# Kernel tuning notes

Measured on AMD Instinct MI355X. Metric: run time of the kernel, lower is better.

## Reference

```python
import jax, jax.numpy as jnp
import numpy as np

B, T, D = 16, 2048, 256
WINDOW = 128


def setup_inputs() -> dict:
    key = jax.random.key(0)
    ks = jax.random.split(key, 6)
    scale = 1.0 / np.sqrt(D)
    return {
        "x": jax.random.normal(ks[0], (B, T, D), dtype=jnp.float32),
        "Wq": jax.random.normal(ks[1], (D, D), dtype=jnp.float32) * scale,
        "Wk": jax.random.normal(ks[2], (D, D), dtype=jnp.float32) * scale,
        "Wv": jax.random.normal(ks[3], (D, D), dtype=jnp.float32) * scale,
        "Wo": jax.random.normal(ks[4], (D, D), dtype=jnp.float32) * scale,
        "w_bias": jax.random.normal(ks[5], (T, T), dtype=jnp.float32) * 0.1,
        "window": WINDOW,
    }


def reference(x, Wq, Wk, Wv, Wo, w_bias, window):
    # x: [B,T,D]; w_bias: [T,T] learned pairwise position bias.
    T_ = x.shape[1]
    q = jnp.einsum("btd,de->bte", x, Wq)
    k = jnp.einsum("btd,de->bte", x, Wk)
    v = jnp.einsum("btd,de->bte", x, Wv)

    # AFT-Local: bias is zeroed outside the local band |t - t'| < window,
    # but ALL positions still contribute (with bias 0) to the weighted sum.
    idx = jnp.arange(T_)
    band = jnp.abs(idx[:, None] - idx[None, :]) < window  # [T,T] bool
    w_local = jnp.where(band, w_bias, 0.0)

    # Stable exponentials: the num/den ratio is invariant to per-row shifts
    # of w and per-(b,d) shifts of k.
    w_stable = w_local - jnp.max(w_local, axis=1, keepdims=True)
    k_stable = k - jnp.max(k, axis=1, keepdims=True)
    expw = jnp.exp(w_stable)  # [T,T]
    expk = jnp.exp(k_stable)  # [B,T,D]

    num = jnp.einsum("ts,bsd->btd", expw, expk * v)
    den = jnp.einsum("ts,bsd->btd", expw, expk)
    y = jax.nn.sigmoid(q) * (num / den)
    return jnp.einsum("btd,de->bte", y, Wo)
```

## Files before the change

kernel.cpp:

```cpp
#include <hip/hip_runtime.h>
#include <math.h>

#define B_ 16
#define T_ 2048
#define D_ 256
#define W_ 128
#define M_ (B_*T_)

typedef __attribute__((ext_vector_type(8))) short bf16x8;
typedef __attribute__((ext_vector_type(4))) float f32x4;
typedef unsigned short u16;

static __device__ __forceinline__ u16 f32_bf16_rne(float f) {
    unsigned int u = __float_as_uint(f);
    u += 0x7FFF + ((u >> 16) & 1);
    return (u16)(u >> 16);
}
static __device__ __forceinline__ float bf16_f32(u16 h) {
    return __uint_as_float(((unsigned int)h) << 16);
}
static __device__ __forceinline__ void gload_lds16(const u16* g, u16* l) {
    __builtin_amdgcn_global_load_lds(
        (const __attribute__((address_space(1))) void*)g,
        (__attribute__((address_space(3))) void*)l, 16, 0, 0);
}

__global__ __launch_bounds__(256) void aft_split_wT(
    const float* __restrict__ Wq, const float* __restrict__ Wk,
    const float* __restrict__ Wv, const float* __restrict__ Wo,
    u16* __restrict__ Wth, u16* __restrict__ Wkl)
{
    __shared__ alignas(16) u16 Th[64][72];
    __shared__ alignas(16) u16 Tl[64][72];
    const float* Ws[4] = {Wq, Wk, Wv, Wo};
    const int mat = blockIdx.x;
    const float* W = Ws[mat];
    const int k0 = (blockIdx.y & 3) * 64;
    const int n0 = (blockIdx.y >> 2) * 64;
    const int tid = threadIdx.x;

    #pragma unroll
    for (int p = 0; p < 4; ++p) {
        const int k = p * 16 + (tid >> 4);
        const int n = (tid & 15) * 4;
        float4 v = *(const float4*)&W[(size_t)(k0 + k) * 256 + n0 + n];
        float vv[4] = {v.x, v.y, v.z, v.w};
        #pragma unroll
        for (int e = 0; e < 4; ++e) {
            u16 h = f32_bf16_rne(vv[e]);
            Th[n + e][k] = h;
            Tl[n + e][k] = f32_bf16_rne(vv[e] - bf16_f32(h));
        }
    }
    __syncthreads();

    const int n  = tid >> 2;
    const int kc = (tid & 3) * 16;
    size_t ob = ((size_t)mat * 256 + n0 + n) * 256 + k0 + kc;
    *(uint4*)&Wth[ob]     = *(const uint4*)&Th[n][kc];
    *(uint4*)&Wth[ob + 8] = *(const uint4*)&Th[n][kc + 8];
    if (mat == 1) {
        size_t ol = ((size_t)(n0 + n)) * 256 + k0 + kc;
        *(uint4*)&Wkl[ol]     = *(const uint4*)&Tl[n][kc];
        *(uint4*)&Wkl[ol + 8] = *(const uint4*)&Tl[n][kc + 8];
    }
}

__global__ void aft_ewb(const float* __restrict__ wb, u16* __restrict__ EWb)
{
    const int t = blockIdx.x;
    const int j = threadIdx.x;
    const int s = (t & ~63) - 128 + j;
    const int dlt = s - t;
    float v = 0.f;
    if (s >= 0 && s < T_ && dlt > -W_ && dlt < W_)
        v = expf(wb[(size_t)t * T_ + s]) - 1.0f;
    EWb[(size_t)t * 320 + j] = f32_bf16_rne(v);
}

__global__ __launch_bounds__(256, 3) void aft_qkv_mfma(
    const float* __restrict__ x,
    const u16* __restrict__ Wth, const u16* __restrict__ Wkl,
    u16* __restrict__ ekT, u16* __restrict__ sigqT)
{
    __shared__ alignas(16) u16 sm[12288];
    u16* Ah = sm;
    u16* Al = sm + 2048;
    u16* Bs = sm + 4096;
    u16* Tr = sm;

    const int tid  = threadIdx.x;
    const int row0 = blockIdx.x * 64;
    const int col0 = blockIdx.y * 64;
    const int b    = row0 >> 11;
    const int t0g  = row0 & (T_ - 1);
    const int lane = tid & 63;
    const int wid  = tid >> 6;
    const int wm   = (wid >> 1) * 32;
    const int wn   = (wid & 1) * 32;
    const int qd   = lane >> 4;
    const int r    = lane & 15;

    f32x4 accq[2][2], acck[2][2], accv[2][2];
    #pragma unroll
    for (int i = 0; i < 2; ++i)
        #pragma unroll
        for (int j = 0; j < 2; ++j) {
            accq[i][j] = (f32x4){0.f, 0.f, 0.f, 0.f};
            acck[i][j] = accq[i][j];
            accv[i][j] = accq[i][j];
        }

    const int crow  = tid >> 2;
    const int gchk  = tid & 3;
    const int cswz  = (crow >> 1) & 3;
    const int ccols = (gchk ^ cswz) * 8;
    const int aslot = crow * 32 + (gchk ^ cswz) * 8;
    const int wbase = wid * 512;
    const int sq8   = (qd ^ ((r >> 1) & 3)) * 8;

    for (int k0 = 0; k0 < D_; k0 += 32) {
        if (k0) __syncthreads();
        {
            size_t gb = (size_t)(col0 + crow) * 256 + k0 + ccols;
            gload_lds16(&Wth[gb],          &Bs[0 * 2048 + wbase]);
            gload_lds16(&Wth[65536 + gb],  &Bs[1 * 2048 + wbase]);
            gload_lds16(&Wkl[gb],          &Bs[2 * 2048 + wbase]);
            gload_lds16(&Wth[131072 + gb], &Bs[3 * 2048 + wbase]);
        }
        {
            size_t ga = (size_t)(row0 + crow) * 256 + k0 + gchk * 8;
            float4 v0 = *(const float4*)&x[ga];
            float4 v1 = *(const float4*)&x[ga + 4];
            float vv[8] = {v0.x, v0.y, v0.z, v0.w, v1.x, v1.y, v1.z, v1.w};
            union { uint4 q; u16 h[8]; } H, L;
            #pragma unroll
            for (int e = 0; e < 8; ++e) {
                u16 h = f32_bf16_rne(vv[e]);
                H.h[e] = h;
                L.h[e] = f32_bf16_rne(vv[e] - bf16_f32(h));
            }
            *(uint4*)&Ah[aslot] = H.q;
            *(uint4*)&Al[aslot] = L.q;
        }
        __syncthreads();

        bf16x8 ah[2], al[2];
        #pragma unroll
        for (int mf = 0; mf < 2; ++mf) {
            int ar = (wm + mf * 16 + r) * 32 + sq8;
            ah[mf] = *(const bf16x8*)&Ah[ar];
            al[mf] = *(const bf16x8*)&Al[ar];
        }
        #pragma unroll
        for (int nf = 0; nf < 2; ++nf) {
            int br = (wn + nf * 16 + r) * 32 + sq8;
            bf16x8 bq  = *(const bf16x8*)&Bs[br];
            bf16x8 bkh = *(const bf16x8*)&Bs[2048 + br];
            bf16x8 bkl = *(const bf16x8*)&Bs[4096 + br];
            bf16x8 bv  = *(const bf16x8*)&Bs[6144 + br];
            #pragma unroll
            for (int mf = 0; mf < 2; ++mf) {
                accq[mf][nf] = __builtin_amdgcn_mfma_f32_16x16x32_bf16(ah[mf], bq,  accq[mf][nf], 0, 0, 0);
                acck[mf][nf] = __builtin_amdgcn_mfma_f32_16x16x32_bf16(ah[mf], bkh, acck[mf][nf], 0, 0, 0);
                acck[mf][nf] = __builtin_amdgcn_mfma_f32_16x16x32_bf16(ah[mf], bkl, acck[mf][nf], 0, 0, 0);
                acck[mf][nf] = __builtin_amdgcn_mfma_f32_16x16x32_bf16(al[mf], bkh, acck[mf][nf], 0, 0, 0);
                accv[mf][nf] = __builtin_amdgcn_mfma_f32_16x16x32_bf16(ah[mf], bv,  accv[mf][nf], 0, 0, 0);
            }
        }
    }

    const int dl_r = tid >> 2;
    const int tseg = (tid & 3) * 16;
    #pragma unroll
    for (int round = 0; round < 3; ++round) {
        __syncthreads();
        #pragma unroll
        for (int mf = 0; mf < 2; ++mf) {
            #pragma unroll
            for (int nf = 0; nf < 2; ++nf) {
                ushort4 o;
                float vals[4];
                #pragma unroll
                for (int reg = 0; reg < 4; ++reg) {
                    if (round == 0)      vals[reg] = expf(acck[mf][nf][reg]);
                    else if (round == 1) vals[reg] = expf(acck[mf][nf][reg]) * accv[mf][nf][reg];
                    else                 vals[reg] = 1.f / (1.f + expf(-accq[mf][nf][reg]));
                }
                o.x = f32_bf16_rne(vals[0]); o.y = f32_bf16_rne(vals[1]);
                o.z = f32_bf16_rne(vals[2]); o.w = f32_bf16_rne(vals[3]);
                int dl = wn + nf * 16 + r;
                int tt = wm + mf * 16 + qd * 4;
                *(ushort4*)&Tr[dl * 72 + tt] = o;
            }
        }
        __syncthreads();
        u16* dst;
        if (round == 0)      dst = ekT   + ((size_t)(b * 512 + col0 + dl_r)) * 2048;
        else if (round == 1) dst = ekT   + ((size_t)(b * 512 + 256 + col0 + dl_r)) * 2048;
        else                 dst = sigqT + ((size_t)(b * 256 + col0 + dl_r)) * 2048;
        dst += t0g + tseg;
        const u16* srcp = &Tr[dl_r * 72 + tseg];
        *(uint4*)&dst[0] = *(const uint4*)&srcp[0];
        *(uint4*)&dst[8] = *(const uint4*)&srcp[8];
    }
}

__global__ __launch_bounds__(256) void aft_sums(
    const u16* __restrict__ ekT, float* __restrict__ Sk, float* __restrict__ Sv)
{
    const int wid  = threadIdx.x >> 6;
    const int lane = threadIdx.x & 63;
    const int row  = blockIdx.x * 4 + wid;
    const int b = row >> 9, n = row & 511;
    const u16* p = ekT + (size_t)row * 2048 + lane * 32;
    float s = 0.f;
    #pragma unroll
    for (int c = 0; c < 4; ++c) {
        union { uint4 v; u16 h[8]; } u;
        u.v = *(const uint4*)&p[c * 8];
        #pragma unroll
        for (int i = 0; i < 8; ++i) s += bf16_f32(u.h[i]);
    }
    #pragma unroll
    for (int off = 32; off >= 1; off >>= 1) s += __shfl_down(s, off, 64);
    if (lane == 0) {
        if (n < 256) Sk[b * 256 + n] = s;
        else         Sv[b * 256 + n - 256] = s;
    }
}

__global__ __launch_bounds__(256) void aft_band_mfma(
    const u16* __restrict__ EWb, const u16* __restrict__ ekT,
    const u16* __restrict__ sigqT,
    const float* __restrict__ Sk, const float* __restrict__ Sv,
    u16* __restrict__ yTD)
{
    __shared__ alignas(16) u16 sm[10240];
    u16* Aw  = sm;
    u16* Bkv = sm + 2048;

    const int tid  = threadIdx.x;
    const int t0   = blockIdx.x * 64;
    const int b    = blockIdx.y >> 1;
    const int dh   = (blockIdx.y & 1) * 128;
    const int lane = tid & 63;
    const int wid  = tid >> 6;
    const int wn   = wid * 32;
    const int qd   = lane >> 4;
    const int r    = lane & 15;

    f32x4 accn[4][2], accd[4][2];
    #pragma unroll
    for (int i = 0; i < 4; ++i)
        #pragma unroll
        for (int j = 0; j < 2; ++j) {
            accn[i][j] = (f32x4){0.f, 0.f, 0.f, 0.f};
            accd[i][j] = (f32x4){0.f, 0.f, 0.f, 0.f};
        }

    const int crow  = tid >> 2;
    const int gchk  = tid & 3;
    const int cswz  = (crow >> 1) & 3;
    const int ccols = (gchk ^ cswz) * 8;
    const int wbase = wid * 512;
    const int sq8   = (qd ^ ((r >> 1) & 3)) * 8;

    for (int c = 0; c < 10; ++c) {
        const int sc = t0 - 128 + c * 32;
        if (sc < 0 || sc >= T_) continue;
        __syncthreads();
        gload_lds16(&EWb[(size_t)(t0 + crow) * 320 + c * 32 + ccols],
                    &Aw[wbase]);
        #pragma unroll
        for (int rr = 0; rr < 4; ++rr) {
            int nl = rr * 64 + crow;
            int n  = (nl < 128) ? (dh + nl) : (256 + dh + nl - 128);
            gload_lds16(&ekT[((size_t)(b * 512) + n) * 2048 + sc + ccols],
                        &Bkv[rr * 2048 + wbase]);
        }
        __syncthreads();

        bf16x8 af[4];
        #pragma unroll
        for (int mf = 0; mf < 4; ++mf)
            af[mf] = *(const bf16x8*)&Aw[(mf * 16 + r) * 32 + sq8];
        #pragma unroll
        for (int nf = 0; nf < 2; ++nf) {
            bf16x8 be = *(const bf16x8*)&Bkv[(wn + nf * 16 + r) * 32 + sq8];
            bf16x8 bv = *(const bf16x8*)&Bkv[(128 + wn + nf * 16 + r) * 32 + sq8];
            #pragma unroll
            for (int mf = 0; mf < 4; ++mf) {
                accd[mf][nf] = __builtin_amdgcn_mfma_f32_16x16x32_bf16(af[mf], be, accd[mf][nf], 0, 0, 0);
                accn[mf][nf] = __builtin_amdgcn_mfma_f32_16x16x32_bf16(af[mf], bv, accn[mf][nf], 0, 0, 0);
            }
        }
    }

    __syncthreads();
    u16* Ly = sm;
    #pragma unroll
    for (int nf = 0; nf < 2; ++nf) {
        const int dl = wn + nf * 16 + r;
        const int d  = dh + dl;
        const float skq = Sk[(b << 8) + d];
        const float svq = Sv[(b << 8) + d];
        #pragma unroll
        for (int mf = 0; mf < 4; ++mf) {
            const int tt = t0 + mf * 16 + qd * 4;
            size_t off = ((size_t)(b << 8) + d) * 2048 + tt;
            ushort4 sg = *(const ushort4*)&sigqT[off];
            float s4[4] = {bf16_f32(sg.x), bf16_f32(sg.y), bf16_f32(sg.z), bf16_f32(sg.w)};
            #pragma unroll
            for (int reg = 0; reg < 4; ++reg) {
                float y = s4[reg] * (svq + accn[mf][nf][reg]) / (skq + accd[mf][nf][reg]);
                Ly[(mf * 16 + qd * 4 + reg) * 136 + dl] = f32_bf16_rne(y);
            }
        }
    }
    __syncthreads();
    {
        const int tl  = tid >> 2;
        const int ds4 = (tid & 3) * 32;
        u16* dst = yTD + ((size_t)b * 2048 + t0 + tl) * 256 + dh + ds4;
        #pragma unroll
        for (int i = 0; i < 4; ++i)
            *(uint4*)&dst[i * 8] = *(const uint4*)&Ly[tl * 136 + ds4 + i * 8];
    }
}

__global__ __launch_bounds__(256) void aft_out_mfma(
    const u16* __restrict__ yTD, const u16* __restrict__ Woth,
    float* __restrict__ out)
{
    __shared__ alignas(16) u16 sm[6144];
    u16* As = sm;
    u16* Bh = sm + 2048;

    const int tid  = threadIdx.x;
    const int row0 = blockIdx.x * 64;
    const int col0 = blockIdx.y * 128;
    const int lane = tid & 63;
    const int wid  = tid >> 6;
    const int wn   = wid * 32;
    const int qd   = lane >> 4;
    const int r    = lane & 15;

    f32x4 acc[4][2];
    #pragma unroll
    for (int i = 0; i < 4; ++i)
        #pragma unroll
        for (int j = 0; j < 2; ++j)
            acc[i][j] = (f32x4){0.f, 0.f, 0.f, 0.f};

    const int crow  = tid >> 2;
    const int gchk  = tid & 3;
    const int cswz  = (crow >> 1) & 3;
    const int ccols = (gchk ^ cswz) * 8;
    const int wbase = wid * 512;
    const int sq8   = (qd ^ ((r >> 1) & 3)) * 8;

    for (int k0 = 0; k0 < D_; k0 += 32) {
        if (k0) __syncthreads();
        gload_lds16(&yTD[(size_t)(row0 + crow) * 256 + k0 + ccols],
                    &As[wbase]);
        gload_lds16(&Woth[(size_t)(col0 + crow) * 256 + k0 + ccols],
                    &Bh[wbase]);
        gload_lds16(&Woth[(size_t)(col0 + 64 + crow) * 256 + k0 + ccols],
                    &Bh[2048 + wbase]);
        __syncthreads();

        bf16x8 af[4];
        #pragma unroll
        for (int mf = 0; mf < 4; ++mf)
            af[mf] = *(const bf16x8*)&As[(mf * 16 + r) * 32 + sq8];
        #pragma unroll
        for (int nf = 0; nf < 2; ++nf) {
            bf16x8 bh = *(const bf16x8*)&Bh[(wn + nf * 16 + r) * 32 + sq8];
            #pragma unroll
            for (int mf = 0; mf < 4; ++mf)
                acc[mf][nf] = __builtin_amdgcn_mfma_f32_16x16x32_bf16(af[mf], bh, acc[mf][nf], 0, 0, 0);
        }
    }

    #pragma unroll
    for (int mf = 0; mf < 4; ++mf)
        #pragma unroll
        for (int nf = 0; nf < 2; ++nf)
            #pragma unroll
            for (int reg = 0; reg < 4; ++reg) {
                int mrow = row0 + mf * 16 + qd * 4 + reg;
                int ncol = col0 + wn + nf * 16 + r;
                out[(size_t)mrow * D_ + ncol] = acc[mf][nf][reg];
            }
}

extern "C" void kernel_launch(void* const* d_in, const int* in_sizes, int n_in,
                              void* d_out, int out_size, void* d_ws, size_t ws_size,
                              hipStream_t stream)
{
    const float* x  = (const float*)d_in[0];
    const float* Wq = (const float*)d_in[1];
    const float* Wk = (const float*)d_in[2];
    const float* Wv = (const float*)d_in[3];
    const float* Wo = (const float*)d_in[4];
    const float* wb = (const float*)d_in[5];

    u16* Wth   = (u16*)d_ws;
    u16* Wkl   = Wth + 262144;
    u16* EWb   = Wkl + 65536;
    u16* ekT   = EWb + 655360;
    u16* sigqT = ekT + 16777216;
    u16* yTD   = sigqT + 8388608;
    float* Sk  = (float*)(yTD + 8388608);
    float* Sv  = Sk + 4096;

    aft_split_wT<<<dim3(4, 16), 256, 0, stream>>>(Wq, Wk, Wv, Wo, Wth, Wkl);
    aft_ewb<<<dim3(T_), 320, 0, stream>>>(wb, EWb);
    aft_qkv_mfma<<<dim3(M_ / 64, 4), 256, 0, stream>>>(x, Wth, Wkl, ekT, sigqT);
    aft_sums<<<dim3(8192 / 4), 256, 0, stream>>>(ekT, Sk, Sv);
    aft_band_mfma<<<dim3(T_ / 64, B_ * 2), 256, 0, stream>>>(EWb, ekT, sigqT, Sk, Sv, yTD);
    aft_out_mfma<<<dim3(M_ / 64, 2), 256, 0, stream>>>(yTD, Wth + 3 * 65536, (float*)d_out);
}
```

Before: 188.9 us.

## Fuse column sums into QKV epilogue and widen band kernel to 128-row tiles

The QKV GEMM epilogue now writes per-tile partial sums of exp(k) and exp(k)*v, so the separate full reread of ekT in the sums kernel becomes a tiny reduction over 32 partials per row. The band kernel goes from 64 to 128 time rows per block with 512 threads. Two wave groups share each loaded ekT/ekv chunk, halving the redundant band loads of K/V. The EWb tile is now loaded with regular vector loads and zero-padded to cover the wider window, at the cost of more LDS per block and more chunk iterations.

```diff
diff --git a/kernel.cpp b/kernel.cpp
--- a/kernel.cpp
+++ b/kernel.cpp
@@ -81,7 +81,7 @@
 __global__ __launch_bounds__(256, 3) void aft_qkv_mfma(
     const float* __restrict__ x,
     const u16* __restrict__ Wth, const u16* __restrict__ Wkl,
-    u16* __restrict__ ekT, u16* __restrict__ sigqT)
+    u16* __restrict__ ekT, u16* __restrict__ sigqT, float* __restrict__ Skp)
 {
     __shared__ alignas(16) u16 sm[12288];
     u16* Ah = sm;
@@ -94,6 +94,7 @@
     const int col0 = blockIdx.y * 64;
     const int b    = row0 >> 11;
     const int t0g  = row0 & (T_ - 1);
+    const int tblk = blockIdx.x & 31;
     const int lane = tid & 63;
     const int wid  = tid >> 6;
     const int wm   = (wid >> 1) * 32;
@@ -201,52 +202,60 @@
         else                 dst = sigqT + ((size_t)(b * 256 + col0 + dl_r)) * 2048;
         dst += t0g + tseg;
         const u16* srcp = &Tr[dl_r * 72 + tseg];
-        *(uint4*)&dst[0] = *(const uint4*)&srcp[0];
-        *(uint4*)&dst[8] = *(const uint4*)&srcp[8];
-    }
-}
-
-__global__ __launch_bounds__(256) void aft_sums(
-    const u16* __restrict__ ekT, float* __restrict__ Sk, float* __restrict__ Sv)
-{
-    const int wid  = threadIdx.x >> 6;
-    const int lane = threadIdx.x & 63;
-    const int row  = blockIdx.x * 4 + wid;
+        uint4 q0 = *(const uint4*)&srcp[0];
+        uint4 q1 = *(const uint4*)&srcp[8];
+        *(uint4*)&dst[0] = q0;
+        *(uint4*)&dst[8] = q1;
+        if (round < 2) {
+            const u16* h0 = (const u16*)&q0;
+            const u16* h1 = (const u16*)&q1;
+            float s = 0.f;
+            #pragma unroll
+            for (int i = 0; i < 8; ++i) s += bf16_f32(h0[i]);
+            #pragma unroll
+            for (int i = 0; i < 8; ++i) s += bf16_f32(h1[i]);
+            s += __shfl_down(s, 1, 64);
+            s += __shfl_down(s, 2, 64);
+            if ((tid & 3) == 0)
+                Skp[((size_t)(b * 512 + round * 256 + col0 + dl_r)) * 32 + tblk] = s;
+        }
+    }
+}
+
+__global__ __launch_bounds__(256) void aft_sums2(
+    const float* __restrict__ Skp, float* __restrict__ Sk, float* __restrict__ Sv)
+{
+    const int row = blockIdx.x * 256 + threadIdx.x;
+    const float* p = Skp + (size_t)row * 32;
+    float s = 0.f;
+    #pragma unroll
+    for (int c = 0; c < 8; ++c) {
+        float4 v = *(const float4*)&p[c * 4];
+        s += v.x; s += v.y; s += v.z; s += v.w;
+    }
     const int b = row >> 9, n = row & 511;
-    const u16* p = ekT + (size_t)row * 2048 + lane * 32;
-    float s = 0.f;
-    #pragma unroll
-    for (int c = 0; c < 4; ++c) {
-        union { uint4 v; u16 h[8]; } u;
-        u.v = *(const uint4*)&p[c * 8];
-        #pragma unroll
-        for (int i = 0; i < 8; ++i) s += bf16_f32(u.h[i]);
-    }
-    #pragma unroll
-    for (int off = 32; off >= 1; off >>= 1) s += __shfl_down(s, off, 64);
-    if (lane == 0) {
-        if (n < 256) Sk[b * 256 + n] = s;
-        else         Sv[b * 256 + n - 256] = s;
-    }
-}
-
-__global__ __launch_bounds__(256) void aft_band_mfma(
+    if (n < 256) Sk[b * 256 + n] = s;
+    else         Sv[b * 256 + n - 256] = s;
+}
+
+__global__ __launch_bounds__(512, 4) void aft_band_mfma(
     const u16* __restrict__ EWb, const u16* __restrict__ ekT,
     const u16* __restrict__ sigqT,
     const float* __restrict__ Sk, const float* __restrict__ Sv,
     u16* __restrict__ yTD)
 {
-    __shared__ alignas(16) u16 sm[10240];
+    __shared__ alignas(16) u16 sm[17408];
     u16* Aw  = sm;
-    u16* Bkv = sm + 2048;
+    u16* Bkv = sm + 4096;
 
     const int tid  = threadIdx.x;
-    const int t0   = blockIdx.x * 64;
+    const int t0   = blockIdx.x * 128;
     const int b    = blockIdx.y >> 1;
     const int dh   = (blockIdx.y & 1) * 128;
     const int lane = tid & 63;
     const int wid  = tid >> 6;
-    const int wn   = wid * 32;
+    const int th   = wid >> 2;
+    const int wn   = (wid & 3) * 32;
     const int qd   = lane >> 4;
     const int r    = lane & 15;
 
@@ -263,28 +272,33 @@
     const int gchk  = tid & 3;
     const int cswz  = (crow >> 1) & 3;
     const int ccols = (gchk ^ cswz) * 8;
+    const int aslot = crow * 32 + (gchk ^ cswz) * 8;
     const int wbase = wid * 512;
     const int sq8   = (qd ^ ((r >> 1) & 3)) * 8;
 
-    for (int c = 0; c < 10; ++c) {
+    const int jbase = 128 - 64 * (crow >> 6);
+
+    for (int c = 0; c < 12; ++c) {
         const int sc = t0 - 128 + c * 32;
         if (sc < 0 || sc >= T_) continue;
         __syncthreads();
-        gload_lds16(&EWb[(size_t)(t0 + crow) * 320 + c * 32 + ccols],
-                    &Aw[wbase]);
-        #pragma unroll
-        for (int rr = 0; rr < 4; ++rr) {
-            int nl = rr * 64 + crow;
-            int n  = (nl < 128) ? (dh + nl) : (256 + dh + nl - 128);
-            gload_lds16(&ekT[((size_t)(b * 512) + n) * 2048 + sc + ccols],
-                        &Bkv[rr * 2048 + wbase]);
+        gload_lds16(&ekT[((size_t)(b * 512) + dh + crow) * 2048 + sc + ccols],
+                    &Bkv[wbase]);
+        gload_lds16(&ekT[((size_t)(b * 512) + 256 + dh + crow) * 2048 + sc + ccols],
+                    &Bkv[4096 + wbase]);
+        {
+            const int j0 = sc - t0 + jbase;
+            uint4 v = (uint4){0u, 0u, 0u, 0u};
+            if (j0 >= 0 && j0 < 320)
+                v = *(const uint4*)&EWb[(size_t)(t0 + crow) * 320 + j0 + gchk * 8];
+            *(uint4*)&Aw[aslot] = v;
         }
         __syncthreads();
 
         bf16x8 af[4];
         #pragma unroll
         for (int mf = 0; mf < 4; ++mf)
-            af[mf] = *(const bf16x8*)&Aw[(mf * 16 + r) * 32 + sq8];
+            af[mf] = *(const bf16x8*)&Aw[(th * 64 + mf * 16 + r) * 32 + sq8];
         #pragma unroll
         for (int nf = 0; nf < 2; ++nf) {
             bf16x8 be = *(const bf16x8*)&Bkv[(wn + nf * 16 + r) * 32 + sq8];
@@ -307,14 +321,14 @@
         const float svq = Sv[(b << 8) + d];
         #pragma unroll
         for (int mf = 0; mf < 4; ++mf) {
-            const int tt = t0 + mf * 16 + qd * 4;
-            size_t off = ((size_t)(b << 8) + d) * 2048 + tt;
+            const int ttl = th * 64 + mf * 16 + qd * 4;
+            size_t off = ((size_t)(b << 8) + d) * 2048 + t0 + ttl;
             ushort4 sg = *(const ushort4*)&sigqT[off];
             float s4[4] = {bf16_f32(sg.x), bf16_f32(sg.y), bf16_f32(sg.z), bf16_f32(sg.w)};
             #pragma unroll
             for (int reg = 0; reg < 4; ++reg) {
                 float y = s4[reg] * (svq + accn[mf][nf][reg]) / (skq + accd[mf][nf][reg]);
-                Ly[(mf * 16 + qd * 4 + reg) * 136 + dl] = f32_bf16_rne(y);
+                Ly[(ttl + reg) * 136 + dl] = f32_bf16_rne(y);
             }
         }
     }
@@ -414,11 +428,12 @@
     u16* yTD   = sigqT + 8388608;
     float* Sk  = (float*)(yTD + 8388608);
     float* Sv  = Sk + 4096;
+    float* Skp = Sv + 4096;
 
     aft_split_wT<<<dim3(4, 16), 256, 0, stream>>>(Wq, Wk, Wv, Wo, Wth, Wkl);
     aft_ewb<<<dim3(T_), 320, 0, stream>>>(wb, EWb);
-    aft_qkv_mfma<<<dim3(M_ / 64, 4), 256, 0, stream>>>(x, Wth, Wkl, ekT, sigqT);
-    aft_sums<<<dim3(8192 / 4), 256, 0, stream>>>(ekT, Sk, Sv);
-    aft_band_mfma<<<dim3(T_ / 64, B_ * 2), 256, 0, stream>>>(EWb, ekT, sigqT, Sk, Sv, yTD);
+    aft_qkv_mfma<<<dim3(M_ / 64, 4), 256, 0, stream>>>(x, Wth, Wkl, ekT, sigqT, Skp);
+    aft_sums2<<<dim3(32), 256, 0, stream>>>(Skp, Sk, Sv);
+    aft_band_mfma<<<dim3(T_ / 128, B_ * 2), 512, 0, stream>>>(EWb, ekT, sigqT, Sk, Sv, yTD);
     aft_out_mfma<<<dim3(M_ / 64, 2), 256, 0, stream>>>(yTD, Wth + 3 * 65536, (float*)d_out);
 }
```

After: 176.4 us. 6.6% less time.
